# Kernel optimization log

Hardware: AMD Instinct MI355X
Metric: run time of the kernel (lower is better)

The kernel has to match this reference:

```python
import jax, jax.numpy as jnp
import numpy as np

NEG_INF = -jnp.inf
BIG_NEG = -1.0e9


def setup_inputs() -> dict:
    key = jax.random.key(0)
    ks = jax.random.split(key, 8)
    B, S, H = 8, 2048, 1024
    x = jax.random.normal(ks[0], (B, S, H), dtype=jnp.float32)
    attention_mask = jax.random.randint(ks[1], (B, S), 0, 2).astype(jnp.bool_)
    # keep first token always valid so no row is fully padded by the pad mask
    attention_mask = attention_mask.at[:, 0].set(True)
    scale = 0.02
    Wq = jax.random.normal(ks[2], (H, H), dtype=jnp.float32) * scale
    bq = jax.random.normal(ks[3], (H,), dtype=jnp.float32) * scale
    Wk = jax.random.normal(ks[4], (H, H), dtype=jnp.float32) * scale
    bk = jax.random.normal(ks[5], (H,), dtype=jnp.float32) * scale
    Wv = jax.random.normal(ks[6], (H, H), dtype=jnp.float32) * scale
    bv = jax.random.normal(ks[7], (H,), dtype=jnp.float32) * scale
    return {"x": x, "attention_mask": attention_mask, "Wq": Wq, "bq": bq,
            "Wk": Wk, "bk": bk, "Wv": Wv, "bv": bv}


def reference(x, attention_mask, Wq, bq, Wk, bk, Wv, bv):
    H = x.shape[-1]
    scale = jnp.sqrt(jnp.float32(H))
    # torch.nn.Linear: x @ W.T + b
    Q = jnp.einsum('bsh,oh->bso', x, Wq) + bq
    K = jnp.einsum('bsh,oh->bso', x, Wk) + bk
    V = jnp.einsum('bsh,oh->bso', x, Wv) + bv
    scores = jnp.einsum('bqh,bkh->bqk', Q, K) / scale  # [B,S,S]
    # faithful to masked_fill(tril(scores)==0, -inf): masks upper triangle
    # AND any lower-triangle score that is exactly zero
    scores = jnp.where(jnp.tril(scores) == 0, NEG_INF, scores)
    pad = attention_mask[:, :, None] & attention_mask[:, None, :]  # [B,S,S]
    scores = jnp.where(pad, scores, NEG_INF)
    # replace -inf with -1e9 (fully-masked rows -> uniform softmax, as in torch)
    scores = jnp.where(jnp.isneginf(scores), BIG_NEG, scores)
    attn = jax.nn.softmax(scores, axis=-1)
    return jnp.einsum('bqk,bkh->bqh', attn, V)
```

## Files before the change

kernel.cpp:

```cpp
#include <hip/hip_runtime.h>
#include <stdint.h>

typedef __bf16 bf16x8 __attribute__((ext_vector_type(8)));
typedef float f32x4 __attribute__((ext_vector_type(4)));

#define BB 8
#define SS 2048
#define HH 1024

#define TILE_B   32768ll
#define NTRI     136
#define BATCH_B  (NTRI * TILE_B)

#define OFF_Q      0ll
#define OFF_K      33554432ll
#define OFF_VTC    67108864ll
#define OFF_MASK   100663296ll
#define OFF_MEANV  100679680ll
#define OFF_VIDX   100712448ll
#define OFF_NV     100777984ll
#define OFF_XSUM   100778048ll
#define OFF_QCTL   100843520ll
#define OFF_QUEUE  100843584ll
#define OFF_TMP    101711872ll
#define OFF_XBF    (OFF_TMP)
#define OFF_WBF    (OFF_TMP + 33554432ll)
#define OFF_SCORES (OFF_TMP + 39845888ll)

__device__ __forceinline__ unsigned short f2bf(float f) {
  unsigned int u = __float_as_uint(f);
  u += 0x7FFFu + ((u >> 16) & 1u);
  return (unsigned short)(u >> 16);
}
__device__ __forceinline__ float bf2f(unsigned short u) {
  return __uint_as_float(((unsigned int)u) << 16);
}

__device__ __forceinline__ void gl_lds16(const void* g, void* l) {
  __builtin_amdgcn_global_load_lds(
      (const __attribute__((address_space(1))) void*)g,
      (__attribute__((address_space(3))) void*)l, 16, 0, 0);
}

__global__ __launch_bounds__(1024) void canon_mask(
    const unsigned char* __restrict__ m, unsigned char* __restrict__ out) {
  __shared__ int cnt[4];
  const int t = threadIdx.x;
  if (t < 4) cnt[t] = 0;
  __syncthreads();
  uint4 v = ((const uint4*)m)[t];
  const unsigned char* pb = (const unsigned char*)&v;
  int loc[4] = {0, 0, 0, 0};
#pragma unroll
  for (int j = 0; j < 16; ++j)
    if (pb[j]) loc[j & 3]++;
#pragma unroll
  for (int r = 0; r < 4; ++r)
    if (loc[r]) atomicAdd(&cnt[r], loc[r]);
  __syncthreads();
  const int c0 = cnt[0], c1 = cnt[1], c2 = cnt[2], c3 = cnt[3];
  unsigned char ob[16];
  if (c0 > 0 && c1 == 0 && c2 == 0 && c3 == 0) {
    const int* mi = (const int*)m;
#pragma unroll
    for (int j = 0; j < 16; ++j) ob[j] = mi[t * 16 + j] ? 1 : 0;
  } else if (c0 == 0 && (c2 > 0 || c3 > 0)) {
    const float* mf = (const float*)m;
#pragma unroll
    for (int j = 0; j < 16; ++j) ob[j] = (mf[t * 16 + j] != 0.0f) ? 1 : 0;
  } else {
#pragma unroll
    for (int j = 0; j < 16; ++j) ob[j] = pb[j] ? 1 : 0;
  }
  ((uint4*)out)[t] = *(const uint4*)ob;
}

__global__ __launch_bounds__(256) void build_compact(
    const unsigned char* __restrict__ mask, int* __restrict__ vidx,
    int* __restrict__ nv, int* __restrict__ qctl, int* __restrict__ queue) {
  const int b = blockIdx.x;
  const int t = threadIdx.x;
  __shared__ int cnt[256];
  __shared__ int totalS;
  const unsigned char* mb = mask + b * SS;
  unsigned char m[8];
  int c = 0;
#pragma unroll
  for (int j = 0; j < 8; ++j) { m[j] = mb[t * 8 + j]; c += m[j] ? 1 : 0; }
  cnt[t] = c;
  __syncthreads();
  int base = 0;
  for (int i = 0; i < t; ++i) base += cnt[i];
  if (t == 255) totalS = base + c;
  int pos = base;
  int* vb = vidx + b * SS;
#pragma unroll
  for (int j = 0; j < 8; ++j) {
    const int s = t * 8 + j;
    if (m[j]) { vb[pos] = s; ++pos; }
  }
  __syncthreads();
  const int total = totalS;
  if (t == 0) {
    nv[b] = total;
    const int ntile = (total + 255) >> 8;
    const int n = ntile * 12;
    const int qb = atomicAdd(&qctl[1], n);
    int k = 0;
    for (int tt = 0; tt < ntile; ++tt)
      for (int z = 0; z < 3; ++z)
        for (int bn = 0; bn < 4; ++bn)
          queue[qb + (k++)] = (((b << 3) | tt) << 4) | (z << 2) | bn;
  }
  for (int idx = total + t; idx < SS; idx += 256) vb[idx] = 0;
}

__global__ void cvt_f32_bf16(const float* __restrict__ in,
                             unsigned short* __restrict__ out, int n4) {
  int i = blockIdx.x * blockDim.x + threadIdx.x;
  int stride = gridDim.x * blockDim.x;
  for (; i < n4; i += stride) {
    float4 v = ((const float4*)in)[i];
    ushort4 o;
    o.x = f2bf(v.x); o.y = f2bf(v.y); o.z = f2bf(v.z); o.w = f2bf(v.w);
    ((ushort4*)out)[i] = o;
  }
}

__global__ void cvt_w3(const float* __restrict__ Wq, const float* __restrict__ Wk,
                       const float* __restrict__ Wv, unsigned short* __restrict__ out) {
  const int z = blockIdx.y;
  const float* src = (z == 0) ? Wq : (z == 1) ? Wk : Wv;
  unsigned short* dst = out + (long)z * (HH * HH);
  const int n4 = HH * HH / 4;
  int i = blockIdx.x * 256 + threadIdx.x;
  for (; i < n4; i += 256 * 256) {
    float4 v = ((const float4*)src)[i];
    ushort4 o;
    o.x = f2bf(v.x); o.y = f2bf(v.y); o.z = f2bf(v.z); o.w = f2bf(v.w);
    ((ushort4*)dst)[i] = o;
  }
}

__global__ __launch_bounds__(256) void xsum_cols(
    const unsigned short* __restrict__ Xbf, float* __restrict__ xsum) {
  const int b = blockIdx.y;
  const int sc = blockIdx.x;
  const int t = threadIdx.x;
  const unsigned short* base = Xbf + ((long)b * SS + sc * 64) * HH + t * 4;
  float s0 = 0.f, s1 = 0.f, s2 = 0.f, s3 = 0.f;
#pragma unroll 4
  for (int i = 0; i < 64; ++i) {
    ushort4 u = *(const ushort4*)(base + (long)i * HH);
    s0 += bf2f(u.x); s1 += bf2f(u.y); s2 += bf2f(u.z); s3 += bf2f(u.w);
  }
  float* xs = xsum + b * HH + t * 4;
  atomicAdd(&xs[0], s0); atomicAdd(&xs[1], s1);
  atomicAdd(&xs[2], s2); atomicAdd(&xs[3], s3);
}

__global__ __launch_bounds__(256) void meanv_dot(
    const float* __restrict__ xsum, const unsigned short* __restrict__ Wvbf,
    const float* __restrict__ bv, float* __restrict__ meanV) {
  const int b = blockIdx.y;
  const int wave = threadIdx.x >> 6, lane = threadIdx.x & 63;
  const int h = blockIdx.x * 4 + wave;
  const unsigned short* wrow = Wvbf + (long)h * HH + lane * 16;
  const float* xs = xsum + b * HH + lane * 16;
  float s = 0.f;
#pragma unroll
  for (int j = 0; j < 4; ++j) {
    ushort4 u = *(const ushort4*)(wrow + j * 4);
    s += bf2f(u.x) * xs[j * 4 + 0] + bf2f(u.y) * xs[j * 4 + 1] +
         bf2f(u.z) * xs[j * 4 + 2] + bf2f(u.w) * xs[j * 4 + 3];
  }
#pragma unroll
  for (int off = 32; off > 0; off >>= 1) s += __shfl_down(s, off, 64);
  if (lane == 0) meanV[(long)b * HH + h] = s + 2048.0f * bv[h];
}

__global__ __launch_bounds__(256) void fixup_masked(
    float* __restrict__ out, const unsigned char* __restrict__ mask,
    const float* __restrict__ sums) {
  const long row = blockIdx.x;
  if (mask[row]) return;
  const long b = row >> 11;
  const int t = threadIdx.x;
  float4 v = ((const float4*)(sums + b * HH))[t];
  v.x *= (1.f / 2048.f); v.y *= (1.f / 2048.f);
  v.z *= (1.f / 2048.f); v.w *= (1.f / 2048.f);
  ((float4*)(out + row * HH))[t] = v;
}

__global__ __launch_bounds__(512, 2) void gemm256q(
    const unsigned short* __restrict__ Abase,
    const unsigned short* __restrict__ Bbase, long bStride,
    char* __restrict__ Cq, char* __restrict__ Ck, char* __restrict__ VtcOut,
    const float* __restrict__ biasq, const float* __restrict__ biask,
    const float* __restrict__ biasv,
    const int* __restrict__ vidx, const int* __restrict__ queue,
    int* __restrict__ qctl) {
  extern __shared__ char smem[];
  int* bc = (int*)(smem + 131072);
  const int tid = threadIdx.x;
  const int wave = tid >> 6, lane = tid & 63;
  const int wr = wave >> 2, wc = wave & 3;
  const int l15 = lane & 15, l4 = lane >> 4;

  const int srow = tid >> 3;
  const int gslot = (tid & 7) ^ (srow & 7);
  const int ldsStageW = wave << 10;
  const int sw0 = ((l4 ^ (l15 & 7)) << 4);
  const int sw1 = (((4 + l4) ^ (l15 & 7)) << 4);
  const int aB0 = (wr << 14) + l15 * 128 + sw0;
  const int aB1 = (wr << 14) + l15 * 128 + sw1;
  const int bB0 = 32768 + ((wc >> 1) << 14) + (((wc & 1) << 6) + l15) * 128 + sw0;
  const int bB1 = 32768 + ((wc >> 1) << 14) + (((wc & 1) << 6) + l15) * 128 + sw1;
  const int rl0 = (wr << 7) + (l4 << 2);
  const int cl0 = (wc << 6) + l15;
  const int qcnt = qctl[1];

  for (;;) {
    __syncthreads();
    if (tid == 0) *bc = atomicAdd(&qctl[0], 1);
    __syncthreads();
    const int idx = *bc;
    if (idx >= qcnt) break;
    const int e = queue[idx];
    const int bm = e >> 4;
    const int bz = (e >> 2) & 3;
    const int bn = e & 3;
    const int b = bm >> 3;
    const int rInB = (bm & 7) * 256;

    const int* vb = vidx + b * SS;
    const char* aS[4];
#pragma unroll
    for (int j = 0; j < 4; ++j) {
      const int r = rInB + srow + 64 * j;
      aS[j] = (const char*)Abase + ((long)b * SS + vb[r]) * 2048 + gslot * 16;
    }
    const char* gB = (const char*)(Bbase + (long)bz * bStride) +
                     ((long)bn * 256 + srow) * 2048 + gslot * 16;

#define STG(kt_, type_, buf_) do { \
    char* _l = smem + ((buf_) << 16) + (((type_) >> 1) << 15) + \
               (((type_) & 1) << 14) + ldsStageW; \
    if ((type_) < 2) { \
      gl_lds16(aS[(type_) * 2]     + ((long)(kt_) << 7), _l); \
      gl_lds16(aS[(type_) * 2 + 1] + ((long)(kt_) << 7), _l + 8192); \
    } else { \
      const char* _g = gB + (((type_) & 1) ? 262144 : 0) + ((long)(kt_) << 7); \
      gl_lds16(_g, _l); \
      gl_lds16(_g + 131072, _l + 8192); \
    } } while (0)

    f32x4 acc[8][4];
    const f32x4 z4 = {0.f, 0.f, 0.f, 0.f};
#pragma unroll
    for (int m = 0; m < 8; ++m)
#pragma unroll
      for (int n = 0; n < 4; ++n) acc[m][n] = z4;

    STG(0, 0, 0); STG(0, 1, 0); STG(0, 2, 0); STG(0, 3, 0);
    STG(1, 0, 1); STG(1, 1, 1); STG(1, 2, 1); STG(1, 3, 1);
    asm volatile("s_waitcnt vmcnt(8)" ::: "memory");
    __builtin_amdgcn_s_barrier();
    __builtin_amdgcn_sched_barrier(0);

    bf16x8 aC[4][2], bLo[2][2], bHi[2][2];

    for (int it = 0; it < 8; ++it) {
#pragma unroll
      for (int g = 0; g < 8; ++g) {
        const int buf = (g < 4) ? 0 : 65536;
        const int q = g & 3;
        if (q == 0) {
#pragma unroll
          for (int mm = 0; mm < 4; ++mm) {
            aC[mm][0] = *(const bf16x8*)(smem + buf + aB0 + mm * 2048);
            aC[mm][1] = *(const bf16x8*)(smem + buf + aB1 + mm * 2048);
          }
#pragma unroll
          for (int nn = 0; nn < 2; ++nn) {
            bLo[nn][0] = *(const bf16x8*)(smem + buf + bB0 + nn * 2048);
            bLo[nn][1] = *(const bf16x8*)(smem + buf + bB1 + nn * 2048);
          }
        } else if (q == 1) {
#pragma unroll
          for (int nn = 0; nn < 2; ++nn) {
            bHi[nn][0] = *(const bf16x8*)(smem + buf + bB0 + (2 + nn) * 2048);
            bHi[nn][1] = *(const bf16x8*)(smem + buf + bB1 + (2 + nn) * 2048);
          }
        } else if (q == 2) {
#pragma unroll
          for (int mm = 0; mm < 4; ++mm) {
            aC[mm][0] = *(const bf16x8*)(smem + buf + aB0 + (4 + mm) * 2048);
            aC[mm][1] = *(const bf16x8*)(smem + buf + aB1 + (4 + mm) * 2048);
          }
        }
        {
          const int u = it * 8 + g - 2;
          if (u >= 0) {
            const int kt = 2 + (u >> 2);
            if (kt < 16) {
              if (g == 0)      STG(kt, 0, 1);
              else if (g == 1) STG(kt, 1, 1);
              else if (g == 2) STG(kt, 2, 0);
              else if (g == 3) STG(kt, 3, 0);
              else if (g == 4) STG(kt, 0, 0);
              else if (g == 5) STG(kt, 1, 0);
              else if (g == 6) STG(kt, 2, 1);
              else             STG(kt, 3, 1);
            }
          }
        }
        __builtin_amdgcn_s_barrier();
        asm volatile("s_waitcnt lgkmcnt(0)" ::: "memory");
        __builtin_amdgcn_sched_barrier(0);
        __builtin_amdgcn_s_setprio(1);
        if (q == 0) {
#pragma unroll
          for (int mm = 0; mm < 4; ++mm)
#pragma unroll
            for (int nn = 0; nn < 2; ++nn) {
              acc[mm][nn] = __builtin_amdgcn_mfma_f32_16x16x32_bf16(
                  aC[mm][0], bLo[nn][0], acc[mm][nn], 0, 0, 0);
              acc[mm][nn] = __builtin_amdgcn_mfma_f32_16x16x32_bf16(
                  aC[mm][1], bLo[nn][1], acc[mm][nn], 0, 0, 0);
            }
        } else if (q == 1) {
#pragma unroll
          for (int mm = 0; mm < 4; ++mm)
#pragma unroll
            for (int nn = 0; nn < 2; ++nn) {
              acc[mm][2 + nn] = __builtin_amdgcn_mfma_f32_16x16x32_bf16(
                  aC[mm][0], bHi[nn][0], acc[mm][2 + nn], 0, 0, 0);
              acc[mm][2 + nn] = __builtin_amdgcn_mfma_f32_16x16x32_bf16(
                  aC[mm][1], bHi[nn][1], acc[mm][2 + nn], 0, 0, 0);
            }
        } else if (q == 2) {
#pragma unroll
          for (int mm = 0; mm < 4; ++mm)
#pragma unroll
            for (int nn = 0; nn < 2; ++nn) {
              acc[4 + mm][2 + nn] = __builtin_amdgcn_mfma_f32_16x16x32_bf16(
                  aC[mm][0], bHi[nn][0], acc[4 + mm][2 + nn], 0, 0, 0);
              acc[4 + mm][2 + nn] = __builtin_amdgcn_mfma_f32_16x16x32_bf16(
                  aC[mm][1], bHi[nn][1], acc[4 + mm][2 + nn], 0, 0, 0);
            }
        } else {
#pragma unroll
          for (int mm = 0; mm < 4; ++mm)
#pragma unroll
            for (int nn = 0; nn < 2; ++nn) {
              acc[4 + mm][nn] = __builtin_amdgcn_mfma_f32_16x16x32_bf16(
                  aC[mm][0], bLo[nn][0], acc[4 + mm][nn], 0, 0, 0);
              acc[4 + mm][nn] = __builtin_amdgcn_mfma_f32_16x16x32_bf16(
                  aC[mm][1], bLo[nn][1], acc[4 + mm][nn], 0, 0, 0);
            }
        }
        __builtin_amdgcn_s_setprio(0);
        __builtin_amdgcn_sched_barrier(0);
        if (q == 3) {
          if (g == 3 && it == 7)
            asm volatile("s_waitcnt vmcnt(0)" ::: "memory");
          else
            asm volatile("s_waitcnt vmcnt(4)" ::: "memory");
        }
        __builtin_amdgcn_s_barrier();
        asm volatile("" ::: "memory");
      }
    }
#undef STG

    if (bz < 2) {
      const float* bias = (bz == 0) ? biasq : biask;
#pragma unroll
      for (int n = 0; n < 4; ++n) {
        const int cl = cl0 + n * 16;
        const float bv = bias[bn * 256 + cl];
        const int colx = cl ^ (l4 << 4);
#pragma unroll
        for (int m = 0; m < 8; ++m) {
          const int rl = rl0 + m * 16;
#pragma unroll
          for (int r = 0; r < 4; ++r)
            *(unsigned short*)(smem + (rl + r) * 512 + colx * 2) =
                f2bf(acc[m][n][r] + bv);
        }
      }
      __syncthreads();
      unsigned short* C = (unsigned short*)((bz == 0) ? Cq : Ck);
      const long rowg0 = (long)b * SS + rInB;
      const long colb0 = (long)bn * 512;
#pragma unroll
      for (int i = 0; i < 16; ++i) {
        const int s2 = i * 512 + tid;
        const int row = s2 >> 5;
        const int cb = s2 & 31;
        const int lb = (row * 512 + (cb << 4)) ^ (((row >> 2) & 3) << 5);
        *(uint4*)((char*)C + (rowg0 + row) * 2048 + colb0 + (cb << 4)) =
            *(const uint4*)(smem + lb);
      }
    } else {
#pragma unroll
      for (int n = 0; n < 4; ++n) {
        const int h = cl0 + n * 16;
        const float bv = biasv[bn * 256 + h];
        const int xr = (h & 7) << 4;
#pragma unroll
        for (int m = 0; m < 8; ++m) {
          const int s0a = rl0 + m * 16;
          uint2 w;
          w.x = (unsigned)f2bf(acc[m][n][0] + bv) |
                ((unsigned)f2bf(acc[m][n][1] + bv) << 16);
          w.y = (unsigned)f2bf(acc[m][n][2] + bv) |
                ((unsigned)f2bf(acc[m][n][3] + bv) << 16);
          *(uint2*)(smem + h * 512 + ((s0a * 2) ^ xr)) = w;
        }
      }
      __syncthreads();
      char* VtB = VtcOut + (long)b * (SS * HH * 2) + (long)(bm & 7) * 512;
#pragma unroll
      for (int i = 0; i < 16; ++i) {
        const int s2 = i * 512 + tid;
        const int h = s2 >> 5;
        const int cb = s2 & 31;
        const int lb = h * 512 + ((cb << 4) ^ ((h & 7) << 4));
        *(uint4*)(VtB + (long)(bn * 256 + h) * 4096 + cb * 16) =
            *(const uint4*)(smem + lb);
      }
    }
  }
}

__global__ __launch_bounds__(256, 2) void gemm128s(
    const unsigned short* __restrict__ Qc, const unsigned short* __restrict__ Kc,
    char* __restrict__ scoresBase, const int* __restrict__ nv) {
  __shared__ __align__(16) char smem[65536];
  const int tid = threadIdx.x;
  const int wave = tid >> 6, lane = tid & 63;
  const int wr = wave >> 1, wc = wave & 1;
  const int l15 = lane & 15, l4 = lane >> 4;
  const int bz = blockIdx.y;

  int t0 = blockIdx.x, bm = 0, a_ = 0;
  while (a_ + bm + 1 <= t0) { ++bm; a_ += bm; }
  const int bn = t0 - a_;

  const int nt = (nv[bz] + 127) >> 7;
  if (bm >= nt) return;

  const unsigned short* A = Qc + (long)bz * SS * HH;
  const unsigned short* B = Kc + (long)bz * SS * HH;

  const int s0 = tid, s1 = tid + 256;
  const int rA0 = ((s0 >> 3) << 1) | (((s0 >> 2) & 1) ^ ((s0 >> 4) & 1));
  const int cA0 = (s0 & 3) ^ (rA0 & 3);
  const int rA1 = ((s1 >> 3) << 1) | (((s1 >> 2) & 1) ^ ((s1 >> 4) & 1));
  const int cA1 = (s1 & 3) ^ (rA1 & 3);
  const char* aG0 = (const char*)A + (long)(bm * 128 + rA0) * 2048 + cA0 * 16;
  const char* aG1 = (const char*)A + (long)(bm * 128 + rA1) * 2048 + cA1 * 16;
  const char* bG0 = (const char*)B + (long)(bn * 128 + rA0) * 2048 + cA0 * 16;
  const char* bG1 = (const char*)B + (long)(bn * 128 + rA1) * 2048 + cA1 * 16;
  const int ldsL0 = wave << 10;
  const int ldsL1 = 4096 + (wave << 10);

#define STG(t_) do { \
    char* _p = smem + (((t_) & 3) << 14); \
    const long _ko = (long)(t_) << 6; \
    gl_lds16(aG0 + _ko, _p + ldsL0); \
    gl_lds16(aG1 + _ko, _p + ldsL1); \
    gl_lds16(bG0 + _ko, _p + 8192 + ldsL0); \
    gl_lds16(bG1 + _ko, _p + 8192 + ldsL1); } while (0)

  const int baseSwz = ((l15 * 64 + (l4 << 4)) ^ ((l15 & 7) << 4));
  const int rdA = (wr << 12) + baseSwz;
  const int rdB = 8192 + (wc << 12) + baseSwz;

  f32x4 acc[4][4];
  const f32x4 z4 = {0.f, 0.f, 0.f, 0.f};
#pragma unroll
  for (int m = 0; m < 4; ++m)
#pragma unroll
    for (int n = 0; n < 4; ++n) acc[m][n] = z4;

  STG(0); STG(1); STG(2);
  asm volatile("s_waitcnt vmcnt(8)" ::: "memory");
  __builtin_amdgcn_s_barrier();
  __builtin_amdgcn_sched_barrier(0);

  const int kT = 32;
  for (int t = 0; t < kT; ++t) {
    if (t + 3 < kT) STG(t + 3);
    const char* bufp = smem + ((t & 3) << 14);
    bf16x8 af[4], bg[4];
#pragma unroll
    for (int m = 0; m < 4; ++m)
      af[m] = *(const bf16x8*)(bufp + rdA + (m << 10));
#pragma unroll
    for (int n = 0; n < 4; ++n)
      bg[n] = *(const bf16x8*)(bufp + rdB + (n << 10));
    __builtin_amdgcn_s_setprio(1);
#pragma unroll
    for (int m = 0; m < 4; ++m)
#pragma unroll
      for (int n = 0; n < 4; ++n)
        acc[m][n] = __builtin_amdgcn_mfma_f32_16x16x32_bf16(af[m], bg[n],
                                                            acc[m][n], 0, 0, 0);
    __builtin_amdgcn_s_setprio(0);
    __builtin_amdgcn_sched_barrier(0);
    if (t + 3 < kT)       asm volatile("s_waitcnt vmcnt(8)" ::: "memory");
    else if (t + 3 == kT) asm volatile("s_waitcnt vmcnt(4)" ::: "memory");
    else if (t + 2 == kT) asm volatile("s_waitcnt vmcnt(0)" ::: "memory");
    if (t + 1 < kT) {
      __builtin_amdgcn_s_barrier();
      __builtin_amdgcn_sched_barrier(0);
      asm volatile("" ::: "memory");
    }
  }
#undef STG

  const int rl0 = (wr << 6) + (l4 << 2);
  const int cl0 = (wc << 6) + l15;
  char* Ct = scoresBase + (long)bz * BATCH_B + (long)t0 * TILE_B;
  __syncthreads();
#pragma unroll
  for (int m = 0; m < 4; ++m)
#pragma unroll
    for (int r = 0; r < 4; ++r) {
      const int ql = rl0 + m * 16 + r;
      const int qg = bm * 128 + ql;
#pragma unroll
      for (int n = 0; n < 4; ++n) {
        const int kg = bn * 128 + cl0 + n * 16;
        const float v = (kg <= qg) ? acc[m][n][r] * 0.03125f : -1.0e9f;
        const int colx = (cl0 + n * 16) ^ (l4 << 4);
        *(unsigned short*)(smem + ql * 256 + colx * 2) = f2bf(v);
      }
    }
  __syncthreads();
#pragma unroll
  for (int i = 0; i < 8; ++i) {
    const int s2 = i * 256 + tid;
    const int row = s2 >> 4;
    const int cb = s2 & 15;
    const int lb = row * 256 + ((cb << 4) ^ (((row >> 2) & 3) << 5));
    *(uint4*)(Ct + (long)row * 256 + (cb << 4)) = *(const uint4*)(smem + lb);
  }
}

__global__ __launch_bounds__(256) void softmax_tri(char* __restrict__ base,
                                                   const int* __restrict__ nv) {
  const int r = blockIdx.x;
  const int bz = blockIdx.y;
  if (r >= nv[bz]) return;
  const int bm = r >> 7;
  const int w = (bm + 1) << 7;
  char* bb = base + (long)bz * BATCH_B +
             (long)(bm * (bm + 1) / 2) * TILE_B + (long)(r & 127) * 256;
  const int t = threadIdx.x;
  const bool act = (t << 3) < w;
  const int bn = t >> 4;
  const int cl = (t << 3) & 127;
  char* slot = bb + (long)bn * TILE_B + (long)cl * 2;
  float v[8];
  float m = -3.0e38f;
  if (act) {
    ushort4 u0 = ((const ushort4*)slot)[0];
    ushort4 u1 = ((const ushort4*)slot)[1];
    v[0] = bf2f(u0.x); v[1] = bf2f(u0.y); v[2] = bf2f(u0.z); v[3] = bf2f(u0.w);
    v[4] = bf2f(u1.x); v[5] = bf2f(u1.y); v[6] = bf2f(u1.z); v[7] = bf2f(u1.w);
#pragma unroll
    for (int k = 0; k < 8; ++k) m = fmaxf(m, v[k]);
  }
  __shared__ float red[8];
#pragma unroll
  for (int off = 32; off > 0; off >>= 1) m = fmaxf(m, __shfl_down(m, off, 64));
  const int wid = t >> 6, lane = t & 63;
  if (lane == 0) red[wid] = m;
  __syncthreads();
  m = fmaxf(fmaxf(red[0], red[1]), fmaxf(red[2], red[3]));
  float e[8];
  float s = 0.f;
  if (act) {
#pragma unroll
    for (int k = 0; k < 8; ++k) { e[k] = __expf(v[k] - m); s += e[k]; }
  }
#pragma unroll
  for (int off = 32; off > 0; off >>= 1) s += __shfl_down(s, off, 64);
  if (lane == 0) red[4 + wid] = s;
  __syncthreads();
  s = red[4] + red[5] + red[6] + red[7];
  const float inv = 1.0f / s;
  if (act) {
    ushort4 o0, o1;
    o0.x = f2bf(e[0] * inv); o0.y = f2bf(e[1] * inv);
    o0.z = f2bf(e[2] * inv); o0.w = f2bf(e[3] * inv);
    o1.x = f2bf(e[4] * inv); o1.y = f2bf(e[5] * inv);
    o1.z = f2bf(e[6] * inv); o1.w = f2bf(e[7] * inv);
    ((ushort4*)slot)[0] = o0;
    ((ushort4*)slot)[1] = o1;
  }
}

__global__ __launch_bounds__(256, 2) void gemm_pv(
    const char* __restrict__ attn, const unsigned short* __restrict__ Vtc,
    float* __restrict__ Out, const int* __restrict__ vidx,
    const int* __restrict__ nv) {
  __shared__ __align__(16) char smem[65536];
  const int tid = threadIdx.x;
  const int wave = tid >> 6, lane = tid & 63;
  const int wr = wave >> 1, wc = wave & 1;
  const int l15 = lane & 15, l4 = lane >> 4;
  const int bz = blockIdx.z;
  const int bm = 15 - blockIdx.x;
  const int bn = blockIdx.y;

  const int nvb = nv[bz];
  const int nt = (nvb + 127) >> 7;
  if (bm >= nt) return;

  const char* Ab = attn + (long)bz * BATCH_B + (long)(bm * (bm + 1) / 2) * TILE_B;
  const unsigned short* B = Vtc + (long)bz * SS * HH;

  const int s0 = tid, s1 = tid + 256;
  const int rA0 = ((s0 >> 3) << 1) | (((s0 >> 2) & 1) ^ ((s0 >> 4) & 1));
  const int cA0 = (s0 & 3) ^ (rA0 & 3);
  const int rA1 = ((s1 >> 3) << 1) | (((s1 >> 2) & 1) ^ ((s1 >> 4) & 1));
  const int cA1 = (s1 & 3) ^ (rA1 & 3);
  const char* aB0 = Ab + (long)rA0 * 256 + cA0 * 16;
  const char* aB1 = Ab + (long)rA1 * 256 + cA1 * 16;
  const char* bG0 = (const char*)(B + (long)(bn * 128 + rA0) * SS) + cA0 * 16;
  const char* bG1 = (const char*)(B + (long)(bn * 128 + rA1) * SS) + cA1 * 16;
  const int ldsL0 = wave << 10;
  const int ldsL1 = 4096 + (wave << 10);

#define STGPV(t_) do { \
    char* _p = smem + (((t_) & 3) << 14); \
    const long _aO = (long)((t_) >> 2) * TILE_B + (long)((t_) & 3) * 64; \
    const long _bO = (long)(t_) << 6; \
    gl_lds16(aB0 + _aO, _p + ldsL0); \
    gl_lds16(aB1 + _aO, _p + ldsL1); \
    gl_lds16(bG0 + _bO, _p + 8192 + ldsL0); \
    gl_lds16(bG1 + _bO, _p + 8192 + ldsL1); } while (0)

  const int baseSwz = ((l15 * 64 + (l4 << 4)) ^ ((l15 & 7) << 4));
  const int rdA = (wr << 12) + baseSwz;
  const int rdB = 8192 + (wc << 12) + baseSwz;

  f32x4 acc[4][4];
  const f32x4 z4 = {0.f, 0.f, 0.f, 0.f};
#pragma unroll
  for (int m = 0; m < 4; ++m)
#pragma unroll
    for (int n = 0; n < 4; ++n) acc[m][n] = z4;

  STGPV(0); STGPV(1); STGPV(2);
  asm volatile("s_waitcnt vmcnt(8)" ::: "memory");
  __builtin_amdgcn_s_barrier();
  __builtin_amdgcn_sched_barrier(0);

  const int kT = (bm + 1) * 4;
  for (int t = 0; t < kT; ++t) {
    if (t + 3 < kT) STGPV(t + 3);
    const char* bufp = smem + ((t & 3) << 14);
    bf16x8 af[4], bg[4];
#pragma unroll
    for (int m = 0; m < 4; ++m)
      af[m] = *(const bf16x8*)(bufp + rdA + (m << 10));
#pragma unroll
    for (int n = 0; n < 4; ++n)
      bg[n] = *(const bf16x8*)(bufp + rdB + (n << 10));
    __builtin_amdgcn_s_setprio(1);
#pragma unroll
    for (int m = 0; m < 4; ++m)
#pragma unroll
      for (int n = 0; n < 4; ++n)
        acc[m][n] = __builtin_amdgcn_mfma_f32_16x16x32_bf16(af[m], bg[n],
                                                            acc[m][n], 0, 0, 0);
    __builtin_amdgcn_s_setprio(0);
    __builtin_amdgcn_sched_barrier(0);
    if (t + 3 < kT)       asm volatile("s_waitcnt vmcnt(8)" ::: "memory");
    else if (t + 3 == kT) asm volatile("s_waitcnt vmcnt(4)" ::: "memory");
    else if (t + 2 == kT) asm volatile("s_waitcnt vmcnt(0)" ::: "memory");
    if (t + 1 < kT) {
      __builtin_amdgcn_s_barrier();
      __builtin_amdgcn_sched_barrier(0);
      asm volatile("" ::: "memory");
    }
  }
#undef STGPV

  const int rl0 = (wr << 6) + (l4 << 2);
  const int cl0 = (wc << 6) + l15;
  __syncthreads();
#pragma unroll
  for (int m = 0; m < 4; ++m)
#pragma unroll
    for (int r = 0; r < 4; ++r) {
      const int ql = rl0 + m * 16 + r;
#pragma unroll
      for (int n = 0; n < 4; ++n) {
        const int colx = (cl0 + n * 16) ^ (l4 << 4);
        *(float*)(smem + ql * 512 + colx * 4) = acc[m][n][r];
      }
    }
  __syncthreads();
  const int* vb = vidx + (long)bz * SS;
#pragma unroll
  for (int i = 0; i < 16; ++i) {
    const int s2 = i * 256 + tid;
    const int row = s2 >> 5;
    const int cb = s2 & 31;
    const int lb = (row * 512 + (cb << 4)) ^ (((row >> 2) & 3) << 6);
    const int crow = bm * 128 + row;
    if (crow < nvb) {
      const int orig = vb[crow];
      *(uint4*)((char*)Out + (((long)bz * SS + orig) * HH) * 4 +
                (long)bn * 512 + (cb << 4)) = *(const uint4*)(smem + lb);
    }
  }
}

extern "C" void kernel_launch(void* const* d_in, const int* in_sizes, int n_in,
                              void* d_out, int out_size, void* d_ws, size_t ws_size,
                              hipStream_t stream) {
  (void)in_sizes; (void)n_in; (void)out_size; (void)ws_size;
  const float* x = (const float*)d_in[0];
  const unsigned char* mask_raw = (const unsigned char*)d_in[1];
  const float* Wq = (const float*)d_in[2];
  const float* bq = (const float*)d_in[3];
  const float* Wk = (const float*)d_in[4];
  const float* bk = (const float*)d_in[5];
  const float* Wv = (const float*)d_in[6];
  const float* bv = (const float*)d_in[7];
  char* ws = (char*)d_ws;

  unsigned short* Xbf = (unsigned short*)(ws + OFF_XBF);
  unsigned short* Wbf = (unsigned short*)(ws + OFF_WBF);
  unsigned short* Qc = (unsigned short*)(ws + OFF_Q);
  unsigned short* Kc = (unsigned short*)(ws + OFF_K);
  unsigned short* Vtc = (unsigned short*)(ws + OFF_VTC);
  unsigned char* mask = (unsigned char*)(ws + OFF_MASK);
  float* meanV = (float*)(ws + OFF_MEANV);
  int* vidx = (int*)(ws + OFF_VIDX);
  int* nv = (int*)(ws + OFF_NV);
  float* xsum = (float*)(ws + OFF_XSUM);
  int* qctl = (int*)(ws + OFF_QCTL);
  int* queue = (int*)(ws + OFF_QUEUE);

  const long MS = (long)BB * SS;

  (void)hipFuncSetAttribute((const void*)gemm256q,
                            hipFuncAttributeMaxDynamicSharedMemorySize, 131088);

  hipMemsetAsync(qctl, 0, 8, stream);
  hipMemsetAsync(xsum, 0, (size_t)BB * HH * 4, stream);
  canon_mask<<<1, 1024, 0, stream>>>(mask_raw, mask);
  build_compact<<<BB, 256, 0, stream>>>(mask, vidx, nv, qctl, queue);

  cvt_f32_bf16<<<2048, 256, 0, stream>>>(x, Xbf, (int)(MS * HH / 4));
  cvt_w3<<<dim3(256, 3), 256, 0, stream>>>(Wq, Wk, Wv, Wbf);

  xsum_cols<<<dim3(32, BB), 256, 0, stream>>>(Xbf, xsum);
  meanv_dot<<<dim3(HH / 4, BB), 256, 0, stream>>>(
      xsum, Wbf + 2 * HH * HH, bv, meanV);

  gemm256q<<<256, 512, 131088, stream>>>(
      Xbf, Wbf, (long)HH * HH,
      (char*)Qc, (char*)Kc, (char*)Vtc, bq, bk, bv, vidx, queue, qctl);

  gemm128s<<<dim3(NTRI, BB), 256, 0, stream>>>(
      Qc, Kc, ws + OFF_SCORES, nv);

  softmax_tri<<<dim3(SS, BB), 256, 0, stream>>>(ws + OFF_SCORES, nv);

  gemm_pv<<<dim3(SS / 128, HH / 128, BB), 256, 0, stream>>>(
      ws + OFF_SCORES, Vtc, (float*)d_out, vidx, nv);

  fixup_masked<<<BB * SS, 256, 0, stream>>>((float*)d_out, mask, meanV);
}
```

Measured before the change: 246.0 us.

## Use persistent work-queue scheduling for score and PV GEMMs

Builds compact per-batch work queues of valid triangular score tiles and PV tiles in build_compact. The PV queue is ordered longest-first. gemm128s and gemm_pv become persistent kernels with 512 blocks that pull tiles through an atomic counter. This avoids launching many blocks that exit early for padded tiles and balances the uneven triangular PV work. In exchange it adds an atomic and extra barriers per tile, and its correctness depends on the queue counters being reset each call.

New measurement: 239.1 us. 1.03x faster.

```diff
diff --git a/kernel.cpp b/kernel.cpp
--- a/kernel.cpp
+++ b/kernel.cpp
@@ -22,6 +22,8 @@
 #define OFF_XSUM   100778048ll
 #define OFF_QCTL   100843520ll
 #define OFF_QUEUE  100843584ll
+#define OFF_SQ     100846656ll
+#define OFF_PQ     100851008ll
 #define OFF_TMP    101711872ll
 #define OFF_XBF    (OFF_TMP)
 #define OFF_WBF    (OFF_TMP + 33554432ll)
@@ -77,7 +79,8 @@
 
 __global__ __launch_bounds__(256) void build_compact(
     const unsigned char* __restrict__ mask, int* __restrict__ vidx,
-    int* __restrict__ nv, int* __restrict__ qctl, int* __restrict__ queue) {
+    int* __restrict__ nv, int* __restrict__ qctl, int* __restrict__ queue,
+    int* __restrict__ sq, int* __restrict__ pq) {
   const int b = blockIdx.x;
   const int t = threadIdx.x;
   __shared__ int cnt[256];
@@ -104,13 +107,29 @@
   if (t == 0) {
     nv[b] = total;
     const int ntile = (total + 255) >> 8;
-    const int n = ntile * 12;
-    const int qb = atomicAdd(&qctl[1], n);
-    int k = 0;
-    for (int tt = 0; tt < ntile; ++tt)
-      for (int z = 0; z < 3; ++z)
-        for (int bn = 0; bn < 4; ++bn)
-          queue[qb + (k++)] = (((b << 3) | tt) << 4) | (z << 2) | bn;
+    {
+      const int n = ntile * 12;
+      const int qb = atomicAdd(&qctl[1], n);
+      int k = 0;
+      for (int tt = 0; tt < ntile; ++tt)
+        for (int z = 0; z < 3; ++z)
+          for (int bn = 0; bn < 4; ++bn)
+            queue[qb + (k++)] = (((b << 3) | tt) << 4) | (z << 2) | bn;
+    }
+    const int nt = (total + 127) >> 7;
+    {
+      const int ntri = nt * (nt + 1) / 2;
+      const int qb = atomicAdd(&qctl[3], ntri);
+      for (int t0 = 0; t0 < ntri; ++t0) sq[qb + t0] = (b << 8) | t0;
+    }
+    {
+      const int n = nt * 8;
+      const int qb = atomicAdd(&qctl[5], n);
+      int k = 0;
+      for (int bm = nt - 1; bm >= 0; --bm)
+        for (int bn = 0; bn < 8; ++bn)
+          pq[qb + (k++)] = (b << 7) | (bm << 3) | bn;
+    }
   }
   for (int idx = total + t; idx < SS; idx += 256) vb[idx] = 0;
 }
@@ -437,35 +456,47 @@
 
 __global__ __launch_bounds__(256, 2) void gemm128s(
     const unsigned short* __restrict__ Qc, const unsigned short* __restrict__ Kc,
-    char* __restrict__ scoresBase, const int* __restrict__ nv) {
+    char* __restrict__ scoresBase, const int* __restrict__ sq,
+    int* __restrict__ qctl) {
   __shared__ __align__(16) char smem[65536];
+  __shared__ int bc;
   const int tid = threadIdx.x;
   const int wave = tid >> 6, lane = tid & 63;
   const int wr = wave >> 1, wc = wave & 1;
   const int l15 = lane & 15, l4 = lane >> 4;
-  const int bz = blockIdx.y;
-
-  int t0 = blockIdx.x, bm = 0, a_ = 0;
-  while (a_ + bm + 1 <= t0) { ++bm; a_ += bm; }
-  const int bn = t0 - a_;
-
-  const int nt = (nv[bz] + 127) >> 7;
-  if (bm >= nt) return;
-
-  const unsigned short* A = Qc + (long)bz * SS * HH;
-  const unsigned short* B = Kc + (long)bz * SS * HH;
 
   const int s0 = tid, s1 = tid + 256;
   const int rA0 = ((s0 >> 3) << 1) | (((s0 >> 2) & 1) ^ ((s0 >> 4) & 1));
   const int cA0 = (s0 & 3) ^ (rA0 & 3);
   const int rA1 = ((s1 >> 3) << 1) | (((s1 >> 2) & 1) ^ ((s1 >> 4) & 1));
   const int cA1 = (s1 & 3) ^ (rA1 & 3);
-  const char* aG0 = (const char*)A + (long)(bm * 128 + rA0) * 2048 + cA0 * 16;
-  const char* aG1 = (const char*)A + (long)(bm * 128 + rA1) * 2048 + cA1 * 16;
-  const char* bG0 = (const char*)B + (long)(bn * 128 + rA0) * 2048 + cA0 * 16;
-  const char* bG1 = (const char*)B + (long)(bn * 128 + rA1) * 2048 + cA1 * 16;
   const int ldsL0 = wave << 10;
   const int ldsL1 = 4096 + (wave << 10);
+  const int baseSwz = ((l15 * 64 + (l4 << 4)) ^ ((l15 & 7) << 4));
+  const int rdA = (wr << 12) + baseSwz;
+  const int rdB = 8192 + (wc << 12) + baseSwz;
+  const int rl0 = (wr << 6) + (l4 << 2);
+  const int cl0 = (wc << 6) + l15;
+  const int qcnt = qctl[3];
+
+  for (;;) {
+    __syncthreads();
+    if (tid == 0) bc = atomicAdd(&qctl[2], 1);
+    __syncthreads();
+    const int idx = bc;
+    if (idx >= qcnt) break;
+    const int e = sq[idx];
+    const int bz = e >> 8;
+    int t0 = e & 255, bm = 0, a_ = 0;
+    while (a_ + bm + 1 <= t0) { ++bm; a_ += bm; }
+    const int bn = t0 - a_;
+
+    const unsigned short* A = Qc + (long)bz * SS * HH;
+    const unsigned short* B = Kc + (long)bz * SS * HH;
+    const char* aG0 = (const char*)A + (long)(bm * 128 + rA0) * 2048 + cA0 * 16;
+    const char* aG1 = (const char*)A + (long)(bm * 128 + rA1) * 2048 + cA1 * 16;
+    const char* bG0 = (const char*)B + (long)(bn * 128 + rA0) * 2048 + cA0 * 16;
+    const char* bG1 = (const char*)B + (long)(bn * 128 + rA1) * 2048 + cA1 * 16;
 
 #define STG(t_) do { \
     char* _p = smem + (((t_) & 3) << 14); \
@@ -475,79 +506,74 @@
     gl_lds16(bG0 + _ko, _p + 8192 + ldsL0); \
     gl_lds16(bG1 + _ko, _p + 8192 + ldsL1); } while (0)
 
-  const int baseSwz = ((l15 * 64 + (l4 << 4)) ^ ((l15 & 7) << 4));
-  const int rdA = (wr << 12) + baseSwz;
-  const int rdB = 8192 + (wc << 12) + baseSwz;
-
-  f32x4 acc[4][4];
-  const f32x4 z4 = {0.f, 0.f, 0.f, 0.f};
-#pragma unroll
-  for (int m = 0; m < 4; ++m)
-#pragma unroll
-    for (int n = 0; n < 4; ++n) acc[m][n] = z4;
-
-  STG(0); STG(1); STG(2);
-  asm volatile("s_waitcnt vmcnt(8)" ::: "memory");
-  __builtin_amdgcn_s_barrier();
-  __builtin_amdgcn_sched_barrier(0);
-
-  const int kT = 32;
-  for (int t = 0; t < kT; ++t) {
-    if (t + 3 < kT) STG(t + 3);
-    const char* bufp = smem + ((t & 3) << 14);
-    bf16x8 af[4], bg[4];
+    f32x4 acc[4][4];
+    const f32x4 z4 = {0.f, 0.f, 0.f, 0.f};
 #pragma unroll
     for (int m = 0; m < 4; ++m)
-      af[m] = *(const bf16x8*)(bufp + rdA + (m << 10));
-#pragma unroll
-    for (int n = 0; n < 4; ++n)
-      bg[n] = *(const bf16x8*)(bufp + rdB + (n << 10));
-    __builtin_amdgcn_s_setprio(1);
+#pragma unroll
+      for (int n = 0; n < 4; ++n) acc[m][n] = z4;
+
+    STG(0); STG(1); STG(2);
+    asm volatile("s_waitcnt vmcnt(8)" ::: "memory");
+    __builtin_amdgcn_s_barrier();
+    __builtin_amdgcn_sched_barrier(0);
+
+    const int kT = 32;
+    for (int t = 0; t < kT; ++t) {
+      if (t + 3 < kT) STG(t + 3);
+      const char* bufp = smem + ((t & 3) << 14);
+      bf16x8 af[4], bg[4];
+#pragma unroll
+      for (int m = 0; m < 4; ++m)
+        af[m] = *(const bf16x8*)(bufp + rdA + (m << 10));
+#pragma unroll
+      for (int n = 0; n < 4; ++n)
+        bg[n] = *(const bf16x8*)(bufp + rdB + (n << 10));
+      __builtin_amdgcn_s_setprio(1);
+#pragma unroll
+      for (int m = 0; m < 4; ++m)
+#pragma unroll
+        for (int n = 0; n < 4; ++n)
+          acc[m][n] = __builtin_amdgcn_mfma_f32_16x16x32_bf16(af[m], bg[n],
+                                                              acc[m][n], 0, 0, 0);
+      __builtin_amdgcn_s_setprio(0);
+      __builtin_amdgcn_sched_barrier(0);
+      if (t + 3 < kT)       asm volatile("s_waitcnt vmcnt(8)" ::: "memory");
+      else if (t + 3 == kT) asm volatile("s_waitcnt vmcnt(4)" ::: "memory");
+      else if (t + 2 == kT) asm volatile("s_waitcnt vmcnt(0)" ::: "memory");
+      if (t + 1 < kT) {
+        __builtin_amdgcn_s_barrier();
+        __builtin_amdgcn_sched_barrier(0);
+        asm volatile("" ::: "memory");
+      }
+    }
+#undef STG
+
+    char* Ct = scoresBase + (long)bz * BATCH_B + (long)t0 * TILE_B;
+    __syncthreads();
 #pragma unroll
     for (int m = 0; m < 4; ++m)
 #pragma unroll
-      for (int n = 0; n < 4; ++n)
-        acc[m][n] = __builtin_amdgcn_mfma_f32_16x16x32_bf16(af[m], bg[n],
-                                                            acc[m][n], 0, 0, 0);
-    __builtin_amdgcn_s_setprio(0);
-    __builtin_amdgcn_sched_barrier(0);
-    if (t + 3 < kT)       asm volatile("s_waitcnt vmcnt(8)" ::: "memory");
-    else if (t + 3 == kT) asm volatile("s_waitcnt vmcnt(4)" ::: "memory");
-    else if (t + 2 == kT) asm volatile("s_waitcnt vmcnt(0)" ::: "memory");
-    if (t + 1 < kT) {
-      __builtin_amdgcn_s_barrier();
-      __builtin_amdgcn_sched_barrier(0);
-      asm volatile("" ::: "memory");
-    }
-  }
-#undef STG
-
-  const int rl0 = (wr << 6) + (l4 << 2);
-  const int cl0 = (wc << 6) + l15;
-  char* Ct = scoresBase + (long)bz * BATCH_B + (long)t0 * TILE_B;
-  __syncthreads();
-#pragma unroll
-  for (int m = 0; m < 4; ++m)
-#pragma unroll
-    for (int r = 0; r < 4; ++r) {
-      const int ql = rl0 + m * 16 + r;
-      const int qg = bm * 128 + ql;
-#pragma unroll
-      for (int n = 0; n < 4; ++n) {
-        const int kg = bn * 128 + cl0 + n * 16;
-        const float v = (kg <= qg) ? acc[m][n][r] * 0.03125f : -1.0e9f;
-        const int colx = (cl0 + n * 16) ^ (l4 << 4);
-        *(unsigned short*)(smem + ql * 256 + colx * 2) = f2bf(v);
-      }
-    }
-  __syncthreads();
-#pragma unroll
-  for (int i = 0; i < 8; ++i) {
-    const int s2 = i * 256 + tid;
-    const int row = s2 >> 4;
-    const int cb = s2 & 15;
-    const int lb = row * 256 + ((cb << 4) ^ (((row >> 2) & 3) << 5));
-    *(uint4*)(Ct + (long)row * 256 + (cb << 4)) = *(const uint4*)(smem + lb);
+      for (int r = 0; r < 4; ++r) {
+        const int ql = rl0 + m * 16 + r;
+        const int qg = bm * 128 + ql;
+#pragma unroll
+        for (int n = 0; n < 4; ++n) {
+          const int kg = bn * 128 + cl0 + n * 16;
+          const float v = (kg <= qg) ? acc[m][n][r] * 0.03125f : -1.0e9f;
+          const int colx = (cl0 + n * 16) ^ (l4 << 4);
+          *(unsigned short*)(smem + ql * 256 + colx * 2) = f2bf(v);
+        }
+      }
+    __syncthreads();
+#pragma unroll
+    for (int i = 0; i < 8; ++i) {
+      const int s2 = i * 256 + tid;
+      const int row = s2 >> 4;
+      const int cb = s2 & 15;
+      const int lb = row * 256 + ((cb << 4) ^ (((row >> 2) & 3) << 5));
+      *(uint4*)(Ct + (long)row * 256 + (cb << 4)) = *(const uint4*)(smem + lb);
+    }
   }
 }
 
@@ -608,34 +634,48 @@
 __global__ __launch_bounds__(256, 2) void gemm_pv(
     const char* __restrict__ attn, const unsigned short* __restrict__ Vtc,
     float* __restrict__ Out, const int* __restrict__ vidx,
-    const int* __restrict__ nv) {
+    const int* __restrict__ nv, const int* __restrict__ pq,
+    int* __restrict__ qctl) {
   __shared__ __align__(16) char smem[65536];
+  __shared__ int bc;
   const int tid = threadIdx.x;
   const int wave = tid >> 6, lane = tid & 63;
   const int wr = wave >> 1, wc = wave & 1;
   const int l15 = lane & 15, l4 = lane >> 4;
-  const int bz = blockIdx.z;
-  const int bm = 15 - blockIdx.x;
-  const int bn = blockIdx.y;
-
-  const int nvb = nv[bz];
-  const int nt = (nvb + 127) >> 7;
-  if (bm >= nt) return;
-
-  const char* Ab = attn + (long)bz * BATCH_B + (long)(bm * (bm + 1) / 2) * TILE_B;
-  const unsigned short* B = Vtc + (long)bz * SS * HH;
 
   const int s0 = tid, s1 = tid + 256;
   const int rA0 = ((s0 >> 3) << 1) | (((s0 >> 2) & 1) ^ ((s0 >> 4) & 1));
   const int cA0 = (s0 & 3) ^ (rA0 & 3);
   const int rA1 = ((s1 >> 3) << 1) | (((s1 >> 2) & 1) ^ ((s1 >> 4) & 1));
   const int cA1 = (s1 & 3) ^ (rA1 & 3);
-  const char* aB0 = Ab + (long)rA0 * 256 + cA0 * 16;
-  const char* aB1 = Ab + (long)rA1 * 256 + cA1 * 16;
-  const char* bG0 = (const char*)(B + (long)(bn * 128 + rA0) * SS) + cA0 * 16;
-  const char* bG1 = (const char*)(B + (long)(bn * 128 + rA1) * SS) + cA1 * 16;
   const int ldsL0 = wave << 10;
   const int ldsL1 = 4096 + (wave << 10);
+  const int baseSwz = ((l15 * 64 + (l4 << 4)) ^ ((l15 & 7) << 4));
+  const int rdA = (wr << 12) + baseSwz;
+  const int rdB = 8192 + (wc << 12) + baseSwz;
+  const int rl0 = (wr << 6) + (l4 << 2);
+  const int cl0 = (wc << 6) + l15;
+  const int qcnt = qctl[5];
+
+  for (;;) {
+    __syncthreads();
+    if (tid == 0) bc = atomicAdd(&qctl[4], 1);
+    __syncthreads();
+    const int idx = bc;
+    if (idx >= qcnt) break;
+    const int e = pq[idx];
+    const int bz = e >> 7;
+    const int bm = (e >> 3) & 15;
+    const int bn = e & 7;
+    const int nvb = nv[bz];
+
+    const char* Ab = attn + (long)bz * BATCH_B +
+                     (long)(bm * (bm + 1) / 2) * TILE_B;
+    const unsigned short* B = Vtc + (long)bz * SS * HH;
+    const char* aB0 = Ab + (long)rA0 * 256 + cA0 * 16;
+    const char* aB1 = Ab + (long)rA1 * 256 + cA1 * 16;
+    const char* bG0 = (const char*)(B + (long)(bn * 128 + rA0) * SS) + cA0 * 16;
+    const char* bG1 = (const char*)(B + (long)(bn * 128 + rA1) * SS) + cA1 * 16;
 
 #define STGPV(t_) do { \
     char* _p = smem + (((t_) & 3) << 14); \
@@ -646,80 +686,75 @@
     gl_lds16(bG0 + _bO, _p + 8192 + ldsL0); \
     gl_lds16(bG1 + _bO, _p + 8192 + ldsL1); } while (0)
 
-  const int baseSwz = ((l15 * 64 + (l4 << 4)) ^ ((l15 & 7) << 4));
-  const int rdA = (wr << 12) + baseSwz;
-  const int rdB = 8192 + (wc << 12) + baseSwz;
-
-  f32x4 acc[4][4];
-  const f32x4 z4 = {0.f, 0.f, 0.f, 0.f};
-#pragma unroll
-  for (int m = 0; m < 4; ++m)
-#pragma unroll
-    for (int n = 0; n < 4; ++n) acc[m][n] = z4;
-
-  STGPV(0); STGPV(1); STGPV(2);
-  asm volatile("s_waitcnt vmcnt(8)" ::: "memory");
-  __builtin_amdgcn_s_barrier();
-  __builtin_amdgcn_sched_barrier(0);
-
-  const int kT = (bm + 1) * 4;
-  for (int t = 0; t < kT; ++t) {
-    if (t + 3 < kT) STGPV(t + 3);
-    const char* bufp = smem + ((t & 3) << 14);
-    bf16x8 af[4], bg[4];
+    f32x4 acc[4][4];
+    const f32x4 z4 = {0.f, 0.f, 0.f, 0.f};
 #pragma unroll
     for (int m = 0; m < 4; ++m)
-      af[m] = *(const bf16x8*)(bufp + rdA + (m << 10));
-#pragma unroll
-    for (int n = 0; n < 4; ++n)
-      bg[n] = *(const bf16x8*)(bufp + rdB + (n << 10));
-    __builtin_amdgcn_s_setprio(1);
+#pragma unroll
+      for (int n = 0; n < 4; ++n) acc[m][n] = z4;
+
+    STGPV(0); STGPV(1); STGPV(2);
+    asm volatile("s_waitcnt vmcnt(8)" ::: "memory");
+    __builtin_amdgcn_s_barrier();
+    __builtin_amdgcn_sched_barrier(0);
+
+    const int kT = (bm + 1) * 4;
+    for (int t = 0; t < kT; ++t) {
+      if (t + 3 < kT) STGPV(t + 3);
+      const char* bufp = smem + ((t & 3) << 14);
+      bf16x8 af[4], bg[4];
+#pragma unroll
+      for (int m = 0; m < 4; ++m)
+        af[m] = *(const bf16x8*)(bufp + rdA + (m << 10));
+#pragma unroll
+      for (int n = 0; n < 4; ++n)
+        bg[n] = *(const bf16x8*)(bufp + rdB + (n << 10));
+      __builtin_amdgcn_s_setprio(1);
+#pragma unroll
+      for (int m = 0; m < 4; ++m)
+#pragma unroll
+        for (int n = 0; n < 4; ++n)
+          acc[m][n] = __builtin_amdgcn_mfma_f32_16x16x32_bf16(af[m], bg[n],
+                                                              acc[m][n], 0, 0, 0);
+      __builtin_amdgcn_s_setprio(0);
+      __builtin_amdgcn_sched_barrier(0);
+      if (t + 3 < kT)       asm volatile("s_waitcnt vmcnt(8)" ::: "memory");
+      else if (t + 3 == kT) asm volatile("s_waitcnt vmcnt(4)" ::: "memory");
+      else if (t + 2 == kT) asm volatile("s_waitcnt vmcnt(0)" ::: "memory");
+      if (t + 1 < kT) {
+        __builtin_amdgcn_s_barrier();
+        __builtin_amdgcn_sched_barrier(0);
+        asm volatile("" ::: "memory");
+      }
+    }
+#undef STGPV
+
+    __syncthreads();
 #pragma unroll
     for (int m = 0; m < 4; ++m)
 #pragma unroll
-      for (int n = 0; n < 4; ++n)
-        acc[m][n] = __builtin_amdgcn_mfma_f32_16x16x32_bf16(af[m], bg[n],
-                                                            acc[m][n], 0, 0, 0);
-    __builtin_amdgcn_s_setprio(0);
-    __builtin_amdgcn_sched_barrier(0);
-    if (t + 3 < kT)       asm volatile("s_waitcnt vmcnt(8)" ::: "memory");
-    else if (t + 3 == kT) asm volatile("s_waitcnt vmcnt(4)" ::: "memory");
-    else if (t + 2 == kT) asm volatile("s_waitcnt vmcnt(0)" ::: "memory");
-    if (t + 1 < kT) {
-      __builtin_amdgcn_s_barrier();
-      __builtin_amdgcn_sched_barrier(0);
-      asm volatile("" ::: "memory");
-    }
-  }
-#undef STGPV
-
-  const int rl0 = (wr << 6) + (l4 << 2);
-  const int cl0 = (wc << 6) + l15;
-  __syncthreads();
-#pragma unroll
-  for (int m = 0; m < 4; ++m)
-#pragma unroll
-    for (int r = 0; r < 4; ++r) {
-      const int ql = rl0 + m * 16 + r;
-#pragma unroll
-      for (int n = 0; n < 4; ++n) {
-        const int colx = (cl0 + n * 16) ^ (l4 << 4);
-        *(float*)(smem + ql * 512 + colx * 4) = acc[m][n][r];
-      }
-    }
-  __syncthreads();
-  const int* vb = vidx + (long)bz * SS;
-#pragma unroll
-  for (int i = 0; i < 16; ++i) {
-    const int s2 = i * 256 + tid;
-    const int row = s2 >> 5;
-    const int cb = s2 & 31;
-    const int lb = (row * 512 + (cb << 4)) ^ (((row >> 2) & 3) << 6);
-    const int crow = bm * 128 + row;
-    if (crow < nvb) {
-      const int orig = vb[crow];
-      *(uint4*)((char*)Out + (((long)bz * SS + orig) * HH) * 4 +
-                (long)bn * 512 + (cb << 4)) = *(const uint4*)(smem + lb);
+      for (int r = 0; r < 4; ++r) {
+        const int ql = rl0 + m * 16 + r;
+#pragma unroll
+        for (int n = 0; n < 4; ++n) {
+          const int colx = (cl0 + n * 16) ^ (l4 << 4);
+          *(float*)(smem + ql * 512 + colx * 4) = acc[m][n][r];
+        }
+      }
+    __syncthreads();
+    const int* vb = vidx + (long)bz * SS;
+#pragma unroll
+    for (int i = 0; i < 16; ++i) {
+      const int s2 = i * 256 + tid;
+      const int row = s2 >> 5;
+      const int cb = s2 & 31;
+      const int lb = (row * 512 + (cb << 4)) ^ (((row >> 2) & 3) << 6);
+      const int crow = bm * 128 + row;
+      if (crow < nvb) {
+        const int orig = vb[crow];
+        *(uint4*)((char*)Out + (((long)bz * SS + orig) * HH) * 4 +
+                  (long)bn * 512 + (cb << 4)) = *(const uint4*)(smem + lb);
+      }
     }
   }
 }
@@ -750,16 +785,18 @@
   float* xsum = (float*)(ws + OFF_XSUM);
   int* qctl = (int*)(ws + OFF_QCTL);
   int* queue = (int*)(ws + OFF_QUEUE);
+  int* sq = (int*)(ws + OFF_SQ);
+  int* pq = (int*)(ws + OFF_PQ);
 
   const long MS = (long)BB * SS;
 
   (void)hipFuncSetAttribute((const void*)gemm256q,
                             hipFuncAttributeMaxDynamicSharedMemorySize, 131088);
 
-  hipMemsetAsync(qctl, 0, 8, stream);
+  hipMemsetAsync(qctl, 0, 32, stream);
   hipMemsetAsync(xsum, 0, (size_t)BB * HH * 4, stream);
   canon_mask<<<1, 1024, 0, stream>>>(mask_raw, mask);
-  build_compact<<<BB, 256, 0, stream>>>(mask, vidx, nv, qctl, queue);
+  build_compact<<<BB, 256, 0, stream>>>(mask, vidx, nv, qctl, queue, sq, pq);
 
   cvt_f32_bf16<<<2048, 256, 0, stream>>>(x, Xbf, (int)(MS * HH / 4));
   cvt_w3<<<dim3(256, 3), 256, 0, stream>>>(Wq, Wk, Wv, Wbf);
@@ -772,13 +809,12 @@
       Xbf, Wbf, (long)HH * HH,
       (char*)Qc, (char*)Kc, (char*)Vtc, bq, bk, bv, vidx, queue, qctl);
 
-  gemm128s<<<dim3(NTRI, BB), 256, 0, stream>>>(
-      Qc, Kc, ws + OFF_SCORES, nv);
+  gemm128s<<<512, 256, 0, stream>>>(Qc, Kc, ws + OFF_SCORES, sq, qctl);
 
   softmax_tri<<<dim3(SS, BB), 256, 0, stream>>>(ws + OFF_SCORES, nv);
 
-  gemm_pv<<<dim3(SS / 128, HH / 128, BB), 256, 0, stream>>>(
-      ws + OFF_SCORES, Vtc, (float*)d_out, vidx, nv);
+  gemm_pv<<<512, 256, 0, stream>>>(
+      ws + OFF_SCORES, Vtc, (float*)d_out, vidx, nv, pq, qctl);
 
   fixup_masked<<<BB * SS, 256, 0, stream>>>((float*)d_out, mask, meanV);
 }
```
